# Kernel tuning notes

Measured on AMD Instinct MI355X. Metric: run time of the kernel, lower is better.

The kernel has to match this reference:

```python
import jax, jax.numpy as jnp
import numpy as np

FS = 16            # fixStride
LAST_RATIO = 0.5
TAUA, TAUB = 10.0, 0.1
TOT_EPOCHS = 100
EPS = 1e-20
SEED = 777


def _safe_norm(diff):
    # ||diff||_2 with subgradient 0 at 0 (matches torch.norm backward at 0)
    sq = jnp.sum(diff * diff, axis=-1)
    d = jnp.sqrt(jnp.where(sq > 0, sq, 1.0))
    return jnp.where(sq > 0, d, 0.0)


def _forward(x, w_score, b_score, att_params, num_graphs, epoch):
    BN, C = x.shape
    B = int(num_graphs)
    N = BN // B
    RES = N - FS + 1                       # rows per graph (unfold1d)
    MAXP = int(np.ceil(N * LAST_RATIO))    # max_pivot_count = ceil(N*last_ratio/init_ratio)

    # --- TopKPool scorer (init_ratio==1.0): permute nodes per graph by desc score
    scores = (x @ w_score + b_score) / jnp.sqrt(jnp.sum(w_score ** 2))
    perm = jnp.argsort(-scores.reshape(B, N), axis=-1, stable=True)      # [B,N]
    xg = jnp.take_along_axis(x.reshape(B, N, C), perm[..., None], axis=1)

    # --- sliding-window edges: row r -> dests r..r+FS-1, src node r
    dst = jnp.arange(RES)[:, None] + jnp.arange(FS)[None, :]             # [RES,FS]
    x_src = xg[:, :RES, :]                                               # [B,RES,C]
    x_dst = xg[:, dst, :]                                                # [B,RES,FS,C]

    # getSM_ei + scatter_softmax over rows: att = [x_s, x_d] @ att_params
    a1, a2 = att_params[:C], att_params[C:]
    sm = jax.nn.softmax((xg @ a1)[:, :RES, None] + (xg @ a2)[:, dst], axis=-1)  # [B,RES,FS]

    # getDM_ei (sigma=1): gaussian-kernel edge distances
    gk = jnp.exp(-_safe_norm(x_src[:, :, None, :] - x_dst) / 2.0) - EPS  # [B,RES,FS]

    # scatterSort: stable descending sort of gk per row
    order = jnp.argsort(-gk, axis=-1, stable=True)
    gk_sort = jnp.take_along_axis(gk, order, axis=-1)
    sm_sort = jnp.take_along_axis(sm, order, axis=-1)

    # per-rank column logits: scatter-sum of sorted attention over rows of each graph
    logits = jnp.broadcast_to(sm_sort.sum(axis=1)[:, None, :], (B, RES, FS))
    logits = logits.at[:, :, 0].set(-jnp.inf)            # mask rank-0 (self edge)

    # gumbel-softmax with annealed temperature
    tau0 = TAUA * (TAUB / TAUA) ** (float(epoch) / TOT_EPOCHS)
    g = jax.random.gumbel(jax.random.key(SEED), (B, RES, FS), jnp.float32)
    gmb = jax.nn.softmax((g + logits) / tau0, axis=-1)

    # per-row threshold and shifted distances (unsorted layout)
    ths = jnp.sum(gk_sort * gmb, axis=-1, keepdims=True)
    shifted = jax.nn.relu(gk - ths)                      # [B,RES,FS]

    # scatter_min over positions 1..FS-1 (position 0 excluded via index redirect)
    delta = (jnp.argmin(shifted[:, :, 1:], axis=-1) + 1).astype(jnp.int32)  # [B,RES]

    # innerLoopStar: follow skip pointers from row 0, up to MAXP pivots
    def chain(delta_g):
        def step(ptr, _):
            valid = ptr < RES
            piv = jnp.where(valid, ptr, -1)
            nxt = jnp.where(valid, ptr + delta_g[jnp.clip(ptr, 0, RES - 1)], jnp.int32(RES))
            return nxt, piv
        _, pivs = jax.lax.scan(step, jnp.int32(0), None, length=MAXP)
        return pivs

    pivots = jax.vmap(chain)(delta)                      # [B,MAXP], -1 padded
    mask = pivots >= 0
    pooled = jnp.take_along_axis(xg, jnp.clip(pivots, 0, N - 1)[..., None], axis=1)
    pooled = pooled * mask[..., None]                    # [B,MAXP,C]
    return pooled, shifted, pivots


def setup_inputs() -> dict:
    key = jax.random.key(0)
    k0, k1, k2, k3 = jax.random.split(key, 4)
    B, N, C = 128, 512, 64
    return {
        "x": jax.random.normal(k0, (B * N, C), jnp.float32),
        "w_score": jax.random.normal(k1, (C,), jnp.float32),
        "b_score": jax.random.normal(k2, (), jnp.float32),
        "att_params": jax.random.normal(k3, (2 * C,), jnp.float32),
        "num_graphs": B,
        "epoch": 10,
    }


def reference(x, w_score, b_score, att_params, num_graphs, epoch):
    return _forward(x, w_score, b_score, att_params, num_graphs, epoch)
```

## Files before the change

kernel.cpp:

```cpp
#include <hip/hip_runtime.h>
#include <math.h>

#define BB 128
#define NN 512
#define CC 64
#define FS 16
#define RES 497
#define MAXP 256
#define BN (BB*NN)
#define GT (BB*RES*FS)
#define WPB 16
#define NCH 32
#define ROWS (WPB+FS-1)
#define PITCH 66
#define GWIN 64
#define GBLK 8

__device__ __forceinline__ unsigned rotl32(unsigned x, int d){ return (x<<d)|(x>>(32-d)); }

__device__ __forceinline__ void threefry777(unsigned x0, unsigned x1, unsigned &o0, unsigned &o1){
  const unsigned ks0 = 0u, ks1 = 777u;
  const unsigned ks2 = 0x1BD11BDAu ^ ks0 ^ ks1;
  x0 += ks0; x1 += ks1;
  x0+=x1; x1=rotl32(x1,13); x1^=x0;
  x0+=x1; x1=rotl32(x1,15); x1^=x0;
  x0+=x1; x1=rotl32(x1,26); x1^=x0;
  x0+=x1; x1=rotl32(x1, 6); x1^=x0;
  x0+=ks1; x1+=ks2+1u;
  x0+=x1; x1=rotl32(x1,17); x1^=x0;
  x0+=x1; x1=rotl32(x1,29); x1^=x0;
  x0+=x1; x1=rotl32(x1,16); x1^=x0;
  x0+=x1; x1=rotl32(x1,24); x1^=x0;
  x0+=ks2; x1+=ks0+2u;
  x0+=x1; x1=rotl32(x1,13); x1^=x0;
  x0+=x1; x1=rotl32(x1,15); x1^=x0;
  x0+=x1; x1=rotl32(x1,26); x1^=x0;
  x0+=x1; x1=rotl32(x1, 6); x1^=x0;
  x0+=ks0; x1+=ks1+3u;
  x0+=x1; x1=rotl32(x1,17); x1^=x0;
  x0+=x1; x1=rotl32(x1,29); x1^=x0;
  x0+=x1; x1=rotl32(x1,16); x1^=x0;
  x0+=x1; x1=rotl32(x1,24); x1^=x0;
  x0+=ks1; x1+=ks2+4u;
  x0+=x1; x1=rotl32(x1,13); x1^=x0;
  x0+=x1; x1=rotl32(x1,15); x1^=x0;
  x0+=x1; x1=rotl32(x1,26); x1^=x0;
  x0+=x1; x1=rotl32(x1, 6); x1^=x0;
  x0+=ks2; x1+=ks0+5u;
  o0 = x0; o1 = x1;
}

__device__ __forceinline__ float gumbel_at_f32(unsigned p){
  unsigned o0, o1;
  threefry777(0u, p, o0, o1);
  unsigned bits = o0 ^ o1;
  float fl = __uint_as_float((bits >> 9) | 0x3f800000u) - 1.0f;
  float u  = fmaxf(1.17549435e-38f, fl);
  return -logf(-logf(u));
}

__device__ __forceinline__ double wave_push_f64(double v, int dstLane){
  int lo = __double2loint(v), hi = __double2hiint(v);
  int plo = __builtin_amdgcn_ds_permute(dstLane<<2, lo);
  int phi = __builtin_amdgcn_ds_permute(dstLane<<2, hi);
  return __hiloint2double(phi, plo);
}

__global__ __launch_bounds__(NN) void k_scoresort(const float* __restrict__ x,
    const float* __restrict__ w, const float* __restrict__ bsc,
    const float* __restrict__ att, double* __restrict__ s1s,
    double* __restrict__ s2s, int* __restrict__ perm){
  int b = blockIdx.x, t = threadIdx.x;
  __shared__ double ss[NN];
  __shared__ int    si[NN];
  __shared__ double l1[NN], l2[NN];

  double wn=0.0, dw=0.0, d1=0.0, d2=0.0;
  #pragma unroll
  for (int c=0;c<CC;c++){ double wv=(double)w[c]; wn += wv*wv; }
  const float4* xr = (const float4*)(x + (size_t)(b*NN+t)*CC);
  #pragma unroll
  for (int q=0;q<CC/4;q++){
    float4 v = xr[q];
    double xv;
    xv=(double)v.x; dw+=xv*(double)w[4*q+0]; d1+=xv*(double)att[4*q+0]; d2+=xv*(double)att[CC+4*q+0];
    xv=(double)v.y; dw+=xv*(double)w[4*q+1]; d1+=xv*(double)att[4*q+1]; d2+=xv*(double)att[CC+4*q+1];
    xv=(double)v.z; dw+=xv*(double)w[4*q+2]; d1+=xv*(double)att[4*q+2]; d2+=xv*(double)att[CC+4*q+2];
    xv=(double)v.w; dw+=xv*(double)w[4*q+3]; d1+=xv*(double)att[4*q+3]; d2+=xv*(double)att[CC+4*q+3];
  }
  double s = (dw + (double)bsc[0]) / sqrt(wn);
  int idx = t;
  l1[t] = d1;
  l2[t] = d2;

  for (int k = 2; k <= NN; k <<= 1){
    bool up = ((t & k) == 0);
    for (int j = k >> 1; j >= 64; j >>= 1){
      ss[t] = s; si[t] = idx;
      __syncthreads();
      double os = ss[t ^ j]; int oi = si[t ^ j];
      bool first = ((t & j) == 0);
      bool cmp = (s > os) || (s == os && idx < oi);
      bool keep = (cmp == (first == up));
      if (!keep){ s = os; idx = oi; }
      __syncthreads();
    }
    #pragma unroll
    for (int j = 32; j > 0; j >>= 1){
      if (j <= (k >> 1)){
        double os = __shfl_xor(s, j, 64);
        int    oi = __shfl_xor(idx, j, 64);
        bool first = ((t & j) == 0);
        bool cmp = (s > os) || (s == os && idx < oi);
        bool keep = (cmp == (first == up));
        if (!keep){ s = os; idx = oi; }
      }
    }
  }
  __syncthreads();
  perm[b*NN + t] = idx;
  s1s[b*NN + t] = l1[idx];
  s2s[b*NN + t] = l2[idx];
}

__global__ __launch_bounds__(256) void k_passA(const float* __restrict__ x,
    const int* __restrict__ perm, const double* __restrict__ s1s,
    const double* __restrict__ s2s, double* __restrict__ gkd,
    unsigned char* __restrict__ rank8, double* __restrict__ partial){
  int b = blockIdx.y, ch = blockIdx.x, tid = threadIdx.x;
  int i0 = ch*WPB;
  int nwin  = min(WPB, RES - i0);
  int nrows = min(ROWS, NN - i0);
  __shared__ float  xs[ROWS*PITCH];
  __shared__ int    pg[ROWS];
  __shared__ double wred[4][FS];

  if (tid < nrows) pg[tid] = perm[b*NN + i0 + tid];
  __syncthreads();
  for (int u = tid; u < nrows*16; u += 256){
    int r = u >> 4, seg = u & 15;
    float4 v = ((const float4*)(x + (size_t)(b*NN + pg[r])*CC))[seg];
    float2* dst = (float2*)&xs[r*PITCH + seg*4];
    dst[0] = make_float2(v.x, v.y);
    dst[1] = make_float2(v.z, v.w);
  }
  __syncthreads();

  int w = tid >> 4, j = tid & 15;
  int lane = tid & 63, gbase = lane & 48, wv = tid >> 6;
  bool act = (w < nwin);
  int i = i0 + w;

  double sq = 0.0;
  const float* rs = &xs[w*PITCH];
  const float* rd = &xs[(w+j)*PITCH];
  #pragma unroll
  for (int c2=0;c2<CC/2;c2++){
    float2 a  = *(const float2*)&rs[2*c2];
    float2 bb = *(const float2*)&rd[2*c2];
    double d0 = (double)a.x - (double)bb.x;
    double d1v= (double)a.y - (double)bb.y;
    sq += d0*d0;
    sq += d1v*d1v;
  }
  double d   = (sq > 0.0) ? sqrt(sq) : 0.0;
  double gkv = exp(-d*0.5) - 1e-20;

  int drow = min(i + j, NN-1);
  double smt = s1s[b*NN + i] + s2s[b*NN + drow];
  double m = smt;
  #pragma unroll
  for (int off=8; off; off>>=1) m = fmax(m, __shfl_xor(m, off, 16));
  double em = exp(smt - m);
  double ssum = em;
  #pragma unroll
  for (int off=8; off; off>>=1) ssum += __shfl_xor(ssum, off, 16);
  double smn = em / ssum;

  int rank = 0;
  #pragma unroll
  for (int k=0;k<16;k++){
    double gkk = __shfl(gkv, gbase + k, 64);
    rank += ((gkk > gkv) || (gkk == gkv && k < j)) ? 1 : 0;
  }

  if (act){
    size_t base = ((size_t)b*RES + i)*FS;
    gkd[base + j]   = gkv;
    rank8[base + j] = (unsigned char)rank;
  }

  double contrib = act ? smn : 0.0;
  double srt = wave_push_f64(contrib, gbase + rank);
  srt += __shfl_xor(srt, 16, 64);
  srt += __shfl_xor(srt, 32, 64);
  if (lane < FS) wred[wv][lane] = srt;
  __syncthreads();
  if (tid < FS){
    partial[((size_t)b*NCH + ch)*FS + tid] =
        wred[0][tid] + wred[1][tid] + wred[2][tid] + wred[3][tid];
  }
}

__global__ __launch_bounds__(1024) void k_gumbel(const double* __restrict__ gkd,
    const unsigned char* __restrict__ rank8, const double* __restrict__ partial,
    const int* __restrict__ epoch_p, float* __restrict__ shifted_out,
    int* __restrict__ delta){
  int b = blockIdx.y, tid = threadIdx.x;
  int win = blockIdx.x*GWIN + (tid >> 4);
  int s = tid & 15;
  int lane = tid & 63, gbase = lane & 48;
  __shared__ double pl[NCH*FS];
  __shared__ double cs[FS];

  if (tid < NCH*FS) pl[tid] = partial[(size_t)b*NCH*FS + tid];
  __syncthreads();
  if (tid < FS){
    double a = 0.0;
    #pragma unroll
    for (int ch=0; ch<NCH; ch++) a += pl[ch*FS + tid];
    cs[tid] = a;
  }
  __syncthreads();

  if (win >= RES) return;
  double tau = 10.0 * pow(0.01, (double)epoch_p[0] / 100.0);
  size_t base = ((size_t)b*RES + win)*FS;

  double z;
  if (s == 0) z = -(double)INFINITY;
  else {
    double g = (double)gumbel_at_f32((unsigned)(base + (unsigned)s));
    z = (g + cs[s]) / tau;
  }
  double m = z;
  #pragma unroll
  for (int off=8; off; off>>=1) m = fmax(m, __shfl_xor(m, off, 16));
  double e = (s == 0) ? 0.0 : exp(z - m);
  double ssum = e;
  #pragma unroll
  for (int off=8; off; off>>=1) ssum += __shfl_xor(ssum, off, 16);
  double gmb = e / ssum;

  double gkv = gkd[base + s];
  int rk = rank8[base + s];
  double gmbr = __shfl(gmb, gbase + rk, 64);
  double ths = gkv * gmbr;
  #pragma unroll
  for (int off=8; off; off>>=1) ths += __shfl_xor(ths, off, 16);

  double shv = fmax(gkv - ths, 0.0);
  shifted_out[base + s] = (float)shv;

  double av = (s == 0) ? (double)INFINITY : shv;
  int ai = s;
  #pragma unroll
  for (int off=8; off; off>>=1){
    double ov = __shfl_xor(av, off, 16);
    int    oi = __shfl_xor(ai, off, 16);
    if (ov < av || (ov == av && oi < ai)){ av = ov; ai = oi; }
  }
  if (s == 0) delta[b*RES + win] = ai;
}

__global__ __launch_bounds__(256) void k_chainpool(const int* __restrict__ delta,
    const int* __restrict__ perm, const float* __restrict__ x,
    float* __restrict__ piv_out, float* __restrict__ pooled){
  int b = blockIdx.x, tid = threadIdx.x;
  __shared__ int tbl[8][512];
  __shared__ int pivS[MAXP];

  for (int i = tid; i < 512; i += 256){
    int v;
    if (i < RES){ v = i + delta[b*RES + i]; if (v > RES) v = RES; }
    else v = RES;
    tbl[0][i] = v;
  }
  __syncthreads();
  #pragma unroll
  for (int k=1;k<8;k++){
    int v0 = tbl[k-1][tid];
    int v1 = tbl[k-1][tid+256];
    tbl[k][tid]     = tbl[k-1][v0];
    tbl[k][tid+256] = tbl[k-1][v1];
    __syncthreads();
  }
  {
    int p = 0;
    #pragma unroll
    for (int k=0;k<8;k++) if ((tid>>k)&1) p = tbl[k][p];
    int piv = (p < RES) ? p : -1;
    pivS[tid] = piv;
    piv_out[b*MAXP + tid] = (float)piv;
  }
  __syncthreads();

  for (int u = tid; u < MAXP*16; u += 256){
    int bp = u >> 4, seg = u & 15;
    int piv = pivS[bp];
    float4 v = make_float4(0.f,0.f,0.f,0.f);
    if (piv >= 0){
      int src = perm[b*NN + piv];
      v = ((const float4*)(x + (size_t)(b*NN + src)*CC))[seg];
    }
    ((float4*)pooled)[(size_t)(b*MAXP + bp)*16 + seg] = v;
  }
}

extern "C" void kernel_launch(void* const* d_in, const int* in_sizes, int n_in,
                              void* d_out, int out_size, void* d_ws, size_t ws_size,
                              hipStream_t stream) {
  (void)in_sizes; (void)n_in; (void)out_size; (void)ws_size;
  const float* x    = (const float*)d_in[0];
  const float* w    = (const float*)d_in[1];
  const float* bsc  = (const float*)d_in[2];
  const float* att  = (const float*)d_in[3];
  const int*   epch = (const int*)d_in[5];

  double* s1s     = (double*)d_ws;
  double* s2s     = s1s + BN;
  double* gkd     = s2s + BN;
  double* partial = gkd + GT;
  int*    perm    = (int*)(partial + (size_t)BB*NCH*FS);
  int*    delta   = perm + BN;
  unsigned char* rank8 = (unsigned char*)(delta + BB*RES);

  float* out_pooled  = (float*)d_out;
  float* out_shifted = out_pooled + BB*MAXP*CC;
  float* out_piv     = out_shifted + (size_t)BB*RES*FS;

  k_scoresort<<<BB, NN, 0, stream>>>(x, w, bsc, att, s1s, s2s, perm);
  k_passA    <<<dim3(NCH, BB), 256, 0, stream>>>(x, perm, s1s, s2s, gkd, rank8, partial);
  k_gumbel   <<<dim3(GBLK, BB), 1024, 0, stream>>>(gkd, rank8, partial, epch, out_shifted, delta);
  k_chainpool<<<BB, 256, 0, stream>>>(delta, perm, x, out_piv, out_pooled);
}
```

Measured before the change: 68.86 us.

## Map one thread per window in gumbel kernel instead of 16-lane groups

The gumbel/shift kernel changes from 16 lanes per window with wave shuffles to one thread per window that loops over all 16 edges in registers. The rank permutation goes through a per-thread LDS scratch row, and the argmin becomes a serial loop. This removes the shuffle-reduction chains and double-precision cross-lane traffic, but each thread now does 16× more serial work (including 15 exps and gumbel hashes), memory accesses become strided per thread (uncoalesced loads and stores of 16 consecutive values), and only about 2×128 blocks of 256 threads are launched, which lowers parallelism.

```diff
diff --git a/kernel.cpp b/kernel.cpp
--- a/kernel.cpp
+++ b/kernel.cpp
@@ -13,8 +13,7 @@
 #define NCH 32
 #define ROWS (WPB+FS-1)
 #define PITCH 66
-#define GWIN 64
-#define GBLK 8
+#define GW2 256
 
 __device__ __forceinline__ unsigned rotl32(unsigned x, int d){ return (x<<d)|(x>>(32-d)); }
 
@@ -202,18 +201,17 @@
   }
 }
 
-__global__ __launch_bounds__(1024) void k_gumbel(const double* __restrict__ gkd,
+__global__ __launch_bounds__(256) void k_gumbel(const double* __restrict__ gkd,
     const unsigned char* __restrict__ rank8, const double* __restrict__ partial,
     const int* __restrict__ epoch_p, float* __restrict__ shifted_out,
     int* __restrict__ delta){
   int b = blockIdx.y, tid = threadIdx.x;
-  int win = blockIdx.x*GWIN + (tid >> 4);
-  int s = tid & 15;
-  int lane = tid & 63, gbase = lane & 48;
+  int win = blockIdx.x*GW2 + tid;
   __shared__ double pl[NCH*FS];
   __shared__ double cs[FS];
-
-  if (tid < NCH*FS) pl[tid] = partial[(size_t)b*NCH*FS + tid];
+  __shared__ double glds[256*17];
+
+  for (int u = tid; u < NCH*FS; u += 256) pl[u] = partial[(size_t)b*NCH*FS + u];
   __syncthreads();
   if (tid < FS){
     double a = 0.0;
@@ -227,40 +225,47 @@
   double tau = 10.0 * pow(0.01, (double)epoch_p[0] / 100.0);
   size_t base = ((size_t)b*RES + win)*FS;
 
-  double z;
-  if (s == 0) z = -(double)INFINITY;
-  else {
+  double gk[FS];
+  #pragma unroll
+  for (int j=0;j<FS;j++) gk[j] = gkd[base + j];
+
+  double z[FS];
+  z[0] = 0.0;
+  #pragma unroll
+  for (int s=1;s<FS;s++){
     double g = (double)gumbel_at_f32((unsigned)(base + (unsigned)s));
-    z = (g + cs[s]) / tau;
-  }
-  double m = z;
-  #pragma unroll
-  for (int off=8; off; off>>=1) m = fmax(m, __shfl_xor(m, off, 16));
-  double e = (s == 0) ? 0.0 : exp(z - m);
-  double ssum = e;
-  #pragma unroll
-  for (int off=8; off; off>>=1) ssum += __shfl_xor(ssum, off, 16);
-  double gmb = e / ssum;
-
-  double gkv = gkd[base + s];
-  int rk = rank8[base + s];
-  double gmbr = __shfl(gmb, gbase + rk, 64);
-  double ths = gkv * gmbr;
-  #pragma unroll
-  for (int off=8; off; off>>=1) ths += __shfl_xor(ths, off, 16);
-
-  double shv = fmax(gkv - ths, 0.0);
-  shifted_out[base + s] = (float)shv;
-
-  double av = (s == 0) ? (double)INFINITY : shv;
-  int ai = s;
-  #pragma unroll
-  for (int off=8; off; off>>=1){
-    double ov = __shfl_xor(av, off, 16);
-    int    oi = __shfl_xor(ai, off, 16);
-    if (ov < av || (ov == av && oi < ai)){ av = ov; ai = oi; }
-  }
-  if (s == 0) delta[b*RES + win] = ai;
+    z[s] = (g + cs[s]) / tau;
+  }
+  double m = z[1];
+  #pragma unroll
+  for (int s=2;s<FS;s++) m = fmax(m, z[s]);
+
+  double e[FS]; double ssum = 0.0;
+  e[0] = 0.0;
+  #pragma unroll
+  for (int s=1;s<FS;s++){ e[s] = exp(z[s] - m); ssum += e[s]; }
+
+  int base17 = tid*17;
+  #pragma unroll
+  for (int j=0;j<FS;j++){
+    int rk = (int)rank8[base + j];
+    glds[base17 + rk] = gk[j];
+  }
+  double ths = 0.0;
+  #pragma unroll
+  for (int s=0;s<FS;s++){
+    ths += glds[base17 + s] * (e[s] / ssum);
+  }
+
+  double bv = 0.0; int bj = 1;
+  #pragma unroll
+  for (int j=0;j<FS;j++){
+    double shv = fmax(gk[j] - ths, 0.0);
+    shifted_out[base + j] = (float)shv;
+    if (j == 1){ bv = shv; bj = 1; }
+    else if (j > 1 && shv < bv){ bv = shv; bj = j; }
+  }
+  delta[b*RES + win] = bj;
 }
 
 __global__ __launch_bounds__(256) void k_chainpool(const int* __restrict__ delta,
@@ -331,6 +336,6 @@
 
   k_scoresort<<<BB, NN, 0, stream>>>(x, w, bsc, att, s1s, s2s, perm);
   k_passA    <<<dim3(NCH, BB), 256, 0, stream>>>(x, perm, s1s, s2s, gkd, rank8, partial);
-  k_gumbel   <<<dim3(GBLK, BB), 1024, 0, stream>>>(gkd, rank8, partial, epch, out_shifted, delta);
+  k_gumbel   <<<dim3((RES + GW2 - 1)/GW2, BB), GW2, 0, stream>>>(gkd, rank8, partial, epch, out_shifted, delta);
   k_chainpool<<<BB, 256, 0, stream>>>(delta, perm, x, out_piv, out_pooled);
 }
```

After: 62.29 us. -9.6%, faster.

## Recompute edge distances in second pass instead of storing gk and rank buffers

Applied to the files above, without the earlier changes.

The pass that computes gaussian edge distances no longer writes per-edge gk (double) and rank arrays to global memory. A second pass, fused with the gumbel step, regathers the permuted rows and recomputes distances and ranks. The gumbel softmax is also factored algebraically as exp(g/tau)*exp(colsum/tau), with the per-column factor precomputed by a tiny kernel. This trades recomputation and an extra gather of x, plus one more launch, for removing about 8 MB of intermediate traffic. Dropping the max subtraction from the softmax risks overflow or underflow in the exponentials.

```diff
diff --git a/kernel.cpp b/kernel.cpp
--- a/kernel.cpp
+++ b/kernel.cpp
@@ -13,8 +13,6 @@
 #define NCH 32
 #define ROWS (WPB+FS-1)
 #define PITCH 66
-#define GWIN 64
-#define GBLK 8
 
 __device__ __forceinline__ unsigned rotl32(unsigned x, int d){ return (x<<d)|(x>>(32-d)); }
 
@@ -123,10 +121,9 @@
   s2s[b*NN + t] = l2[idx];
 }
 
-__global__ __launch_bounds__(256) void k_passA(const float* __restrict__ x,
+__global__ __launch_bounds__(256) void k_passA1(const float* __restrict__ x,
     const int* __restrict__ perm, const double* __restrict__ s1s,
-    const double* __restrict__ s2s, double* __restrict__ gkd,
-    unsigned char* __restrict__ rank8, double* __restrict__ partial){
+    const double* __restrict__ s2s, double* __restrict__ partial){
   int b = blockIdx.y, ch = blockIdx.x, tid = threadIdx.x;
   int i0 = ch*WPB;
   int nwin  = min(WPB, RES - i0);
@@ -184,12 +181,6 @@
     rank += ((gkk > gkv) || (gkk == gkv && k < j)) ? 1 : 0;
   }
 
-  if (act){
-    size_t base = ((size_t)b*RES + i)*FS;
-    gkd[base + j]   = gkv;
-    rank8[base + j] = (unsigned char)rank;
-  }
-
   double contrib = act ? smn : 0.0;
   double srt = wave_push_f64(contrib, gbase + rank);
   srt += __shfl_xor(srt, 16, 64);
@@ -202,65 +193,97 @@
   }
 }
 
-__global__ __launch_bounds__(1024) void k_gumbel(const double* __restrict__ gkd,
-    const unsigned char* __restrict__ rank8, const double* __restrict__ partial,
+__global__ void k_ks(const double* __restrict__ partial, const int* __restrict__ epoch_p,
+                     double* __restrict__ Ks){
+  int t = blockIdx.x*blockDim.x + threadIdx.x;
+  if (t >= BB*FS) return;
+  int b = t >> 4, s = t & 15;
+  double a = 0.0;
+  #pragma unroll
+  for (int ch=0; ch<NCH; ch++) a += partial[((size_t)b*NCH + ch)*FS + s];
+  double tau = 10.0 * exp(-4.605170185988091 * ((double)epoch_p[0] / 100.0));
+  Ks[t] = (s == 0) ? 0.0 : exp(a / tau);
+}
+
+__global__ __launch_bounds__(256) void k_passA2(const float* __restrict__ x,
+    const int* __restrict__ perm, const double* __restrict__ Ks,
     const int* __restrict__ epoch_p, float* __restrict__ shifted_out,
     int* __restrict__ delta){
-  int b = blockIdx.y, tid = threadIdx.x;
-  int win = blockIdx.x*GWIN + (tid >> 4);
-  int s = tid & 15;
+  int b = blockIdx.y, ch = blockIdx.x, tid = threadIdx.x;
+  int i0 = ch*WPB;
+  int nwin  = min(WPB, RES - i0);
+  int nrows = min(ROWS, NN - i0);
+  __shared__ float  xs[ROWS*PITCH];
+  __shared__ int    pg[ROWS];
+
+  if (tid < nrows) pg[tid] = perm[b*NN + i0 + tid];
+  __syncthreads();
+  for (int u = tid; u < nrows*16; u += 256){
+    int r = u >> 4, seg = u & 15;
+    float4 v = ((const float4*)(x + (size_t)(b*NN + pg[r])*CC))[seg];
+    float2* dst = (float2*)&xs[r*PITCH + seg*4];
+    dst[0] = make_float2(v.x, v.y);
+    dst[1] = make_float2(v.z, v.w);
+  }
+  __syncthreads();
+
+  int w = tid >> 4, j = tid & 15;
   int lane = tid & 63, gbase = lane & 48;
-  __shared__ double pl[NCH*FS];
-  __shared__ double cs[FS];
-
-  if (tid < NCH*FS) pl[tid] = partial[(size_t)b*NCH*FS + tid];
-  __syncthreads();
-  if (tid < FS){
-    double a = 0.0;
-    #pragma unroll
-    for (int ch=0; ch<NCH; ch++) a += pl[ch*FS + tid];
-    cs[tid] = a;
-  }
-  __syncthreads();
-
-  if (win >= RES) return;
-  double tau = 10.0 * pow(0.01, (double)epoch_p[0] / 100.0);
-  size_t base = ((size_t)b*RES + win)*FS;
-
-  double z;
-  if (s == 0) z = -(double)INFINITY;
-  else {
-    double g = (double)gumbel_at_f32((unsigned)(base + (unsigned)s));
-    z = (g + cs[s]) / tau;
-  }
-  double m = z;
-  #pragma unroll
-  for (int off=8; off; off>>=1) m = fmax(m, __shfl_xor(m, off, 16));
-  double e = (s == 0) ? 0.0 : exp(z - m);
-  double ssum = e;
-  #pragma unroll
-  for (int off=8; off; off>>=1) ssum += __shfl_xor(ssum, off, 16);
-  double gmb = e / ssum;
-
-  double gkv = gkd[base + s];
-  int rk = rank8[base + s];
-  double gmbr = __shfl(gmb, gbase + rk, 64);
-  double ths = gkv * gmbr;
-  #pragma unroll
-  for (int off=8; off; off>>=1) ths += __shfl_xor(ths, off, 16);
+  bool act = (w < nwin);
+  int i = i0 + w;
+
+  double sq = 0.0;
+  const float* rs = &xs[w*PITCH];
+  const float* rd = &xs[(w+j)*PITCH];
+  #pragma unroll
+  for (int c2=0;c2<CC/2;c2++){
+    float2 a  = *(const float2*)&rs[2*c2];
+    float2 bb = *(const float2*)&rd[2*c2];
+    double d0 = (double)a.x - (double)bb.x;
+    double d1v= (double)a.y - (double)bb.y;
+    sq += d0*d0;
+    sq += d1v*d1v;
+  }
+  double d   = (sq > 0.0) ? sqrt(sq) : 0.0;
+  double gkv = exp(-d*0.5) - 1e-20;
+
+  int rank = 0;
+  #pragma unroll
+  for (int k=0;k<16;k++){
+    double gkk = __shfl(gkv, gbase + k, 64);
+    rank += ((gkk > gkv) || (gkk == gkv && k < j)) ? 1 : 0;
+  }
+
+  double tau = 10.0 * exp(-4.605170185988091 * ((double)epoch_p[0] / 100.0));
+  size_t base = ((size_t)b*RES + i)*FS;
+  double Ej = 0.0;
+  if (j != 0){
+    float g = gumbel_at_f32((unsigned)(base + (unsigned)j));
+    Ej = exp((double)g / tau) * Ks[b*FS + j];
+  }
+  double ssumE = Ej;
+  #pragma unroll
+  for (int off=8; off; off>>=1) ssumE += __shfl_xor(ssumE, off, 16);
+
+  double gk_sorted = wave_push_f64(gkv, gbase + rank);
+  double thsp = gk_sorted * (Ej / ssumE);
+  #pragma unroll
+  for (int off=8; off; off>>=1) thsp += __shfl_xor(thsp, off, 16);
+  double ths = thsp;
 
   double shv = fmax(gkv - ths, 0.0);
-  shifted_out[base + s] = (float)shv;
-
-  double av = (s == 0) ? (double)INFINITY : shv;
-  int ai = s;
+  double av = (j == 0) ? (double)INFINITY : shv;
+  int ai = j;
   #pragma unroll
   for (int off=8; off; off>>=1){
     double ov = __shfl_xor(av, off, 16);
     int    oi = __shfl_xor(ai, off, 16);
     if (ov < av || (ov == av && oi < ai)){ av = ov; ai = oi; }
   }
-  if (s == 0) delta[b*RES + win] = ai;
+  if (act){
+    shifted_out[base + j] = (float)shv;
+    if (j == 0) delta[b*RES + i] = ai;
+  }
 }
 
 __global__ __launch_bounds__(256) void k_chainpool(const int* __restrict__ delta,
@@ -319,18 +342,18 @@
 
   double* s1s     = (double*)d_ws;
   double* s2s     = s1s + BN;
-  double* gkd     = s2s + BN;
-  double* partial = gkd + GT;
-  int*    perm    = (int*)(partial + (size_t)BB*NCH*FS);
+  double* partial = s2s + BN;
+  double* Ks      = partial + (size_t)BB*NCH*FS;
+  int*    perm    = (int*)(Ks + BB*FS);
   int*    delta   = perm + BN;
-  unsigned char* rank8 = (unsigned char*)(delta + BB*RES);
 
   float* out_pooled  = (float*)d_out;
   float* out_shifted = out_pooled + BB*MAXP*CC;
   float* out_piv     = out_shifted + (size_t)BB*RES*FS;
 
   k_scoresort<<<BB, NN, 0, stream>>>(x, w, bsc, att, s1s, s2s, perm);
-  k_passA    <<<dim3(NCH, BB), 256, 0, stream>>>(x, perm, s1s, s2s, gkd, rank8, partial);
-  k_gumbel   <<<dim3(GBLK, BB), 1024, 0, stream>>>(gkd, rank8, partial, epch, out_shifted, delta);
+  k_passA1   <<<dim3(NCH, BB), 256, 0, stream>>>(x, perm, s1s, s2s, partial);
+  k_ks       <<<(BB*FS+255)/256, 256, 0, stream>>>(partial, epch, Ks);
+  k_passA2   <<<dim3(NCH, BB), 256, 0, stream>>>(x, perm, Ks, epch, out_shifted, delta);
   k_chainpool<<<BB, 256, 0, stream>>>(delta, perm, x, out_piv, out_pooled);
 }
```

After: 81.43 us. 1.18x slower.
